# Performance work log

Hardware: AMD Instinct MI355X
Metric: run time of the kernel (lower is better)

Reference implementation:

```python
import jax, jax.numpy as jnp
import numpy as np

B, NJ, NM = 64, 30, 20
N = NJ * NM          # 600 operation nodes per FJSP instance
IN_DIM, H = 2, 128


def _bn(h):
    # torch BatchNorm1d in training mode, gamma=1/beta=0 (module init), stats over all nodes
    m = h.mean(axis=(0, 1))
    v = h.var(axis=(0, 1))
    return (h - m) / jnp.sqrt(v + 1e-5)


def setup_inputs() -> dict:
    key = jax.random.key(0)
    ks = jax.random.split(key, 20)
    x = jax.random.normal(ks[0], (B, N, IN_DIM), jnp.float32)
    graph_pool = jnp.full((B, N), 1.0 / N, jnp.float32)   # average graph pooling weights
    padded_nei = jnp.zeros((1,), jnp.int32)               # unused (sum pooling path)
    adj = (jax.random.uniform(ks[1], (B, N, N)) < 0.01).astype(jnp.float32)
    adj = jnp.minimum(adj + jnp.eye(N, dtype=jnp.float32)[None], 1.0)  # self-loops
    candidate = jax.random.randint(ks[2], (B, NJ), 0, N)
    a_index = jax.random.randint(ks[3], (B,), 0, NJ)
    mask = jax.random.uniform(ks[4], (B, NJ)) < 0.2
    mask = mask.at[jnp.arange(B), a_index].set(False)     # chosen action never masked
    mask_mch = jax.random.uniform(ks[5], (B, N, NM)) < 0.3
    dur = jax.random.uniform(ks[6], (B, N, NM), dtype=jnp.float32)
    old_action = jax.random.randint(ks[7], (B,), 0, N)
    mch_pool = jax.random.normal(ks[8], (B, H), jnp.float32)

    def w(k, i, o):
        return jax.random.normal(k, (i, o), jnp.float32) * (1.0 / np.sqrt(i))

    z = lambda n: jnp.zeros((n,), jnp.float32)            # biases init to 0 in module
    return dict(
        x=x, graph_pool=graph_pool, padded_nei=padded_nei, adj=adj,
        candidate=candidate, mask=mask, mask_mch=mask_mch, dur=dur,
        a_index=a_index, old_action=old_action, mch_pool=mch_pool,
        W1_0=w(ks[9], IN_DIM, H), b1_0=z(H), W2_0=w(ks[10], H, H), b2_0=z(H),
        W1_1=w(ks[11], H, H), b1_1=z(H), W2_1=w(ks[12], H, H), b2_1=z(H),
        Wa1=w(ks[13], 3 * H, H), ba1=z(H), Wa2=w(ks[14], H, H), ba2=z(H),
        Wa3=w(ks[15], H, 1), ba3=z(1),
        Wc1=w(ks[16], H, H), bc1=z(H), Wc2=w(ks[17], H, 1), bc2=z(1),
    )


def reference(x, graph_pool, padded_nei, adj, candidate, mask, mask_mch, dur,
              a_index, old_action, mch_pool,
              W1_0, b1_0, W2_0, b2_0, W1_1, b1_1, W2_1, b2_1,
              Wa1, ba1, Wa2, ba2, Wa3, ba3, Wc1, bc1, Wc2, bc2):
    # --- GIN encoder: num_layers-1 = 2 message-passing layers, sum pooling ---
    h = x
    for (W1, b1, W2, b2) in ((W1_0, b1_0, W2_0, b2_0), (W1_1, b1_1, W2_1, b2_1)):
        pooled = jnp.einsum('bnm,bmd->bnd', adj, h)         # neighbor sum (adj has self-loops)
        h1 = jax.nn.relu(_bn(pooled @ W1 + b1))             # MLP hidden (BN inside MLP)
        h = jax.nn.relu(_bn(h1 @ W2 + b2))                  # layer BN + relu
    h_nodes = h                                             # [B, N, H]
    h_pooled = jnp.einsum('bn,bnd->bd', graph_pool, h_nodes)  # [B, H]

    # --- gather candidate features, concat pooled contexts ---
    cand_feat = jnp.take_along_axis(h_nodes, candidate[:, :, None], axis=1)  # [B, NJ, H]
    concat = jnp.concatenate([
        cand_feat,
        jnp.broadcast_to(h_pooled[:, None, :], cand_feat.shape),
        jnp.broadcast_to(mch_pool[:, None, :], cand_feat.shape)], axis=-1)   # [B, NJ, 3H]

    # --- MLPActor(3 layers, tanh) ---
    a = jnp.tanh(concat @ Wa1 + ba1)
    a = jnp.tanh(a @ Wa2 + ba2)
    scores = (a @ Wa3 + ba3).squeeze(-1) * 10.0             # [B, NJ]
    scores = jnp.where(mask, -jnp.inf, scores)
    logpi = jax.nn.log_softmax(scores, axis=1)
    pi = jnp.exp(logpi)
    log_a = jnp.take_along_axis(logpi, a_index[:, None], axis=1)[:, 0]
    entropy = -jnp.sum(jnp.where(pi > 0, pi * logpi, 0.0), axis=1)

    # --- gather action-dependent tensors (detached in torch) ---
    b_idx = jnp.arange(B)
    action_node = dur[b_idx, old_action]                    # [B, NM]
    action_feature = h_nodes[b_idx, old_action]             # [B, H]
    mask_mch_action = mask_mch[b_idx, old_action][:, None, :]  # [B, 1, NM]

    # --- MLPCritic(2 layers, tanh) ---
    v = jnp.tanh(h_pooled @ Wc1 + bc1) @ Wc2 + bc2          # [B, 1]

    sg = jax.lax.stop_gradient
    return (entropy, v, log_a, sg(action_node), sg(action_feature),
            mask_mch_action, sg(h_pooled))
```

## Files before the change

kernel.cpp:

```cpp
#include <hip/hip_runtime.h>
#include <hip/hip_bf16.h>

#define BB 64
#define NJ 30
#define NM 20
#define NN 600
#define HH 128
#define NROWS (BB*NN)
#define CAP 48

typedef __attribute__((ext_vector_type(8))) short short8;
typedef __attribute__((ext_vector_type(4))) float f32x4;

#define STATS_B   0
#define HPOOL_B   4096
#define FLAGS_B   36864
#define ZERO_B    36880
#define WTB_B     37120
#define SCORES_B  135424
#define NBRCNT_B  143104
#define NBRIDX_B  296704
#define POOLED0_B 7669504
#define T1_B      7976704
#define P1_B      27637504

#define OUT_ENT   0
#define OUT_V     64
#define OUT_LOGA  128
#define OUT_ANODE 192
#define OUT_AFEAT 1472
#define OUT_MMCH  9664
#define OUT_HPOOL 10944

__device__ __forceinline__ bool mask_at(const void* p, int layout, long i) {
    if (layout == 2) return ((const float*)p)[i] != 0.f;
    if (layout == 1) return ((const unsigned char*)p)[i] != 0;
    return ((const int*)p)[i] != 0;
}

__device__ __forceinline__ short bf16rne(float f) {
    unsigned u = __float_as_uint(f);
    return (short)((u + 0x7fffu + ((u >> 16) & 1u)) >> 16);
}
__device__ __forceinline__ float bf2f(unsigned h) {
    return __uint_as_float(h << 16);
}
__device__ __forceinline__ unsigned packbf(float a, float b) {
    return ((unsigned)(unsigned short)bf16rne(a)) |
           (((unsigned)(unsigned short)bf16rne(b)) << 16);
}

__global__ __launch_bounds__(256) void k_sparse(const float* __restrict__ adj,
                                                const float* __restrict__ x,
                                                int* __restrict__ nbr_cnt,
                                                int* __restrict__ nbr_idx,
                                                float* __restrict__ pooled0,
                                                const void* mask_p, const void* maskmch_p,
                                                int* flags,
                                                const float* __restrict__ Wa,
                                                const float* __restrict__ Wb,
                                                const float* __restrict__ Wc,
                                                unsigned short* __restrict__ wT) {
    int bid = blockIdx.x;
    int tid = threadIdx.x;
    if (bid < 289) {
        if (bid >= 97) {
            int bid2 = bid - 97;
            int mat = bid2 >> 6;
            int idx = ((bid2 & 63) << 8) + tid;
            const float* W = mat == 0 ? Wa : (mat == 1 ? Wb : Wc);
            int k = idx >> 7, c = idx & 127;
            wT[mat * 16384 + c * HH + k] = (unsigned short)bf16rne(W[idx]);
        } else {
            unsigned agg = 0;
            int which;
            if (bid == 0) {
                which = 0;
                const unsigned* p = (const unsigned*)mask_p;
                unsigned w0 = (tid < 480) ? p[tid] : 0u;
                unsigned w1 = (tid + 256 < 480) ? p[tid + 256] : 0u;
                agg = w0 | w1;
            } else {
                which = 1;
                const unsigned* p = (const unsigned*)maskmch_p + (size_t)(bid - 1) * 200;
                agg = (tid < 200) ? p[tid] : 0u;
            }
            int f = 0;
            if (((agg >> 24) & 0xffu) == 0x3fu) f |= 1;
            if ((((agg >> 8) & 0xffu) == 1u) || (((agg >> 16) & 0xffu) == 1u) ||
                (((agg >> 24) & 0xffu) == 1u)) f |= 2;
#pragma unroll
            for (int off = 1; off < 64; off <<= 1) f |= __shfl_xor(f, off);
            if ((tid & 63) == 0 && f) atomicOr(&flags[which], f);
        }
    }

    int wrow = bid * 4 + (tid >> 6);
    int lane = tid & 63;
    int b = wrow / NN;
    const float4* arow = (const float4*)(adj + (size_t)wrow * NN);
    int* irow = nbr_idx + (size_t)wrow * CAP;
    const float* xb = x + (size_t)b * NN * 2;
    float4 vv[3];
    vv[0] = arow[lane];
    vv[1] = arow[64 + lane];
    vv[2] = (128 + lane < 150) ? arow[128 + lane] : make_float4(0.f, 0.f, 0.f, 0.f);
    int cnt = 0;
    float p0 = 0.f, p1 = 0.f;
#pragma unroll
    for (int it = 0; it < 3; ++it) {
        float4 v = vv[it];
        int col0 = it * 256 + lane * 4;
        bool m0 = v.x != 0.f, m1 = v.y != 0.f, m2 = v.z != 0.f, m3 = v.w != 0.f;
        int c_lane = (int)m0 + (int)m1 + (int)m2 + (int)m3;
        int inc = c_lane;
#pragma unroll
        for (int off = 1; off < 64; off <<= 1) {
            int t = __shfl_up(inc, off);
            if (lane >= off) inc += t;
        }
        int pos = cnt + inc - c_lane;
        if (m0) {
            if (pos < CAP) irow[pos] = col0;
            float2 xv = *(const float2*)&xb[col0 * 2];
            p0 += xv.x; p1 += xv.y; ++pos;
        }
        if (m1) {
            if (pos < CAP) irow[pos] = col0 + 1;
            float2 xv = *(const float2*)&xb[(col0 + 1) * 2];
            p0 += xv.x; p1 += xv.y; ++pos;
        }
        if (m2) {
            if (pos < CAP) irow[pos] = col0 + 2;
            float2 xv = *(const float2*)&xb[(col0 + 2) * 2];
            p0 += xv.x; p1 += xv.y; ++pos;
        }
        if (m3) {
            if (pos < CAP) irow[pos] = col0 + 3;
            float2 xv = *(const float2*)&xb[(col0 + 3) * 2];
            p0 += xv.x; p1 += xv.y; ++pos;
        }
        cnt += __shfl(inc, 63);
    }
#pragma unroll
    for (int off = 1; off < 64; off <<= 1) {
        p0 += __shfl_xor(p0, off);
        p1 += __shfl_xor(p1, off);
    }
    if (lane == 0) {
        nbr_cnt[wrow] = cnt < CAP ? cnt : CAP;
        pooled0[(size_t)wrow * 2]     = p0;
        pooled0[(size_t)wrow * 2 + 1] = p1;
    }
}

__global__ __launch_bounds__(256) void k_p0stats(const float* __restrict__ pooled0,
                                                 float* __restrict__ out5) {
    __shared__ float red[4][5];
    int i = blockIdx.x * 256 + threadIdx.x;
    float p0 = pooled0[(size_t)i * 2], p1 = pooled0[(size_t)i * 2 + 1];
    float v[5] = {p0, p1, p0 * p0, p1 * p1, p0 * p1};
#pragma unroll
    for (int j = 0; j < 5; ++j)
#pragma unroll
        for (int off = 1; off < 64; off <<= 1) v[j] += __shfl_xor(v[j], off);
    int lane = threadIdx.x & 63, w = threadIdx.x >> 6;
    if (lane == 0)
#pragma unroll
        for (int j = 0; j < 5; ++j) red[w][j] = v[j];
    __syncthreads();
    if (threadIdx.x == 0)
#pragma unroll
        for (int j = 0; j < 5; ++j)
            atomicAdd(&out5[j], red[0][j] + red[1][j] + red[2][j] + red[3][j]);
}

template<int MODE>
__global__ __launch_bounds__(256) void k_stage(const void* __restrict__ t_in_v,
                                               const float* __restrict__ pooled0,
                                               const float* __restrict__ W1,
                                               const unsigned short* __restrict__ wT,
                                               const float* __restrict__ stats_in,
                                               unsigned short* __restrict__ t_out,
                                               float* __restrict__ stats_out) {
    __shared__ float sm_mean[HH], sm_inv[HH];
    __shared__ float smS[4][32], smQ[4][32];
    int tid = threadIdx.x;
    if (MODE == 0 && tid < HH) {
        float S0 = stats_in[0], S1 = stats_in[1], Q0 = stats_in[2], Q1 = stats_in[3], P01 = stats_in[4];
        float w0 = W1[tid], w1 = W1[HH + tid];
        float m = (S0 * w0 + S1 * w1) * (1.f / NROWS);
        float eq = (Q0 * w0 * w0 + Q1 * w1 * w1 + 2.f * P01 * w0 * w1) * (1.f / NROWS);
        sm_mean[tid] = m;
        sm_inv[tid] = 1.f / sqrtf(eq - m * m + 1e-5f);
    }
    if (MODE == 1 && tid < HH) {
        float s = stats_in[tid], q = stats_in[HH + tid];
        float m = s * (1.f / NROWS);
        sm_mean[tid] = m;
        sm_inv[tid] = 1.f / sqrtf(q * (1.f / NROWS) - m * m + 1e-5f);
    }
    if (MODE != 2) __syncthreads();

    const unsigned short* tin = (const unsigned short*)t_in_v;
    int lane = tid & 63, wave = tid >> 6;
    int r16 = lane & 15, kg = lane >> 4;
    int rowbase = (blockIdx.x >> 2) * 64 + wave * 16;
    int colq = blockIdx.x & 3;

    f32x4 acc[2];
#pragma unroll
    for (int t = 0; t < 2; ++t)
#pragma unroll
        for (int i = 0; i < 4; ++i) acc[t][i] = 0.f;

    float p0 = 0.f, p1 = 0.f;
    if (MODE == 0) {
        p0 = pooled0[(size_t)(rowbase + r16) * 2];
        p1 = pooled0[(size_t)(rowbase + r16) * 2 + 1];
    }

#pragma unroll
    for (int ks = 0; ks < 4; ++ks) {
        int kb = ks * 32 + kg * 8;
        short8 afr;
        if (MODE == 2) {
            afr = *(const short8*)&tin[(size_t)(rowbase + r16) * HH + kb];
        } else {
            float av[8];
            if (MODE == 0) {
                float4 wa0 = *(const float4*)&W1[kb];
                float4 wa1 = *(const float4*)&W1[kb + 4];
                float4 wb0 = *(const float4*)&W1[HH + kb];
                float4 wb1 = *(const float4*)&W1[HH + kb + 4];
                av[0] = p0 * wa0.x + p1 * wb0.x; av[1] = p0 * wa0.y + p1 * wb0.y;
                av[2] = p0 * wa0.z + p1 * wb0.z; av[3] = p0 * wa0.w + p1 * wb0.w;
                av[4] = p0 * wa1.x + p1 * wb1.x; av[5] = p0 * wa1.y + p1 * wb1.y;
                av[6] = p0 * wa1.z + p1 * wb1.z; av[7] = p0 * wa1.w + p1 * wb1.w;
            } else {
                short8 raw = *(const short8*)&tin[(size_t)(rowbase + r16) * HH + kb];
#pragma unroll
                for (int j = 0; j < 8; ++j) av[j] = bf2f((unsigned short)raw[j]);
            }
            float4 m0 = *(const float4*)&sm_mean[kb];
            float4 m1 = *(const float4*)&sm_mean[kb + 4];
            float4 i0 = *(const float4*)&sm_inv[kb];
            float4 i1 = *(const float4*)&sm_inv[kb + 4];
            av[0] = fmaxf((av[0] - m0.x) * i0.x, 0.f);
            av[1] = fmaxf((av[1] - m0.y) * i0.y, 0.f);
            av[2] = fmaxf((av[2] - m0.z) * i0.z, 0.f);
            av[3] = fmaxf((av[3] - m0.w) * i0.w, 0.f);
            av[4] = fmaxf((av[4] - m1.x) * i1.x, 0.f);
            av[5] = fmaxf((av[5] - m1.y) * i1.y, 0.f);
            av[6] = fmaxf((av[6] - m1.z) * i1.z, 0.f);
            av[7] = fmaxf((av[7] - m1.w) * i1.w, 0.f);
#pragma unroll
            for (int j = 0; j < 8; ++j) afr[j] = bf16rne(av[j]);
        }
#pragma unroll
        for (int t = 0; t < 2; ++t) {
            short8 bfr = *(const short8*)&wT[(size_t)((colq * 2 + t) * 16 + r16) * HH + kb];
            acc[t] = __builtin_amdgcn_mfma_f32_16x16x32_bf16(afr, bfr, acc[t], 0, 0, 0);
        }
    }

#pragma unroll
    for (int t = 0; t < 2; ++t) {
        int lc = t * 16 + r16;
        int col = colq * 32 + lc;
        float s = 0.f, q = 0.f;
#pragma unroll
        for (int i = 0; i < 4; ++i) {
            float v = acc[t][i];
            t_out[(size_t)(rowbase + kg * 4 + i) * HH + col] = (unsigned short)bf16rne(v);
            s += v; q += v * v;
        }
        s += __shfl_xor(s, 16); q += __shfl_xor(q, 16);
        s += __shfl_xor(s, 32); q += __shfl_xor(q, 32);
        if (kg == 0) { smS[wave][lc] = s; smQ[wave][lc] = q; }
    }
    __syncthreads();
    if (tid < 32) {
        int col = colq * 32 + tid;
        atomicAdd(&stats_out[col],      smS[0][tid] + smS[1][tid] + smS[2][tid] + smS[3][tid]);
        atomicAdd(&stats_out[HH + col], smQ[0][tid] + smQ[1][tid] + smQ[2][tid] + smQ[3][tid]);
    }
}

__global__ __launch_bounds__(256) void k_pool1(const unsigned short* __restrict__ t1,
                                               const int* __restrict__ nbr_cnt,
                                               const int* __restrict__ nbr_idx,
                                               const float* __restrict__ stats1,
                                               unsigned short* __restrict__ pooled1) {
    __shared__ float sm_mean[HH], sm_inv[HH];
    int tid = threadIdx.x;
    if (tid < HH) {
        float s = stats1[tid], q = stats1[HH + tid];
        float m = s * (1.f / NROWS);
        sm_mean[tid] = m;
        sm_inv[tid] = 1.f / sqrtf(q * (1.f / NROWS) - m * m + 1e-5f);
    }
    __syncthreads();
    int c4 = tid & 31, rl = tid >> 5;
    int row = blockIdx.x * 8 + rl;
    int b = row / NN;
    float4 mm = *(const float4*)&sm_mean[c4 * 4];
    float4 iv = *(const float4*)&sm_inv[c4 * 4];
    int cnt = nbr_cnt[row];
    const int* ir = nbr_idx + (size_t)row * CAP;
    const unsigned short* tb = t1 + (size_t)b * NN * HH;
    float a0 = 0.f, a1 = 0.f, a2 = 0.f, a3 = 0.f;
    int i = 0;
    for (; i + 1 < cnt; i += 2) {
        int m0 = ir[i], m1 = ir[i + 1];
        uint2 w0 = *(const uint2*)&tb[(size_t)m0 * HH + c4 * 4];
        uint2 w1 = *(const uint2*)&tb[(size_t)m1 * HH + c4 * 4];
        a0 += fmaxf((bf2f(w0.x & 0xffffu) - mm.x) * iv.x, 0.f)
            + fmaxf((bf2f(w1.x & 0xffffu) - mm.x) * iv.x, 0.f);
        a1 += fmaxf((bf2f(w0.x >> 16)     - mm.y) * iv.y, 0.f)
            + fmaxf((bf2f(w1.x >> 16)     - mm.y) * iv.y, 0.f);
        a2 += fmaxf((bf2f(w0.y & 0xffffu) - mm.z) * iv.z, 0.f)
            + fmaxf((bf2f(w1.y & 0xffffu) - mm.z) * iv.z, 0.f);
        a3 += fmaxf((bf2f(w0.y >> 16)     - mm.w) * iv.w, 0.f)
            + fmaxf((bf2f(w1.y >> 16)     - mm.w) * iv.w, 0.f);
    }
    if (i < cnt) {
        int m0 = ir[i];
        uint2 w0 = *(const uint2*)&tb[(size_t)m0 * HH + c4 * 4];
        a0 += fmaxf((bf2f(w0.x & 0xffffu) - mm.x) * iv.x, 0.f);
        a1 += fmaxf((bf2f(w0.x >> 16)     - mm.y) * iv.y, 0.f);
        a2 += fmaxf((bf2f(w0.y & 0xffffu) - mm.z) * iv.z, 0.f);
        a3 += fmaxf((bf2f(w0.y >> 16)     - mm.w) * iv.w, 0.f);
    }
    uint2 o;
    o.x = packbf(a0, a1);
    o.y = packbf(a2, a3);
    *(uint2*)&pooled1[(size_t)row * HH + c4 * 4] = o;
}

__global__ __launch_bounds__(256) void k_hpool(const unsigned short* __restrict__ t3,
                                               const float* __restrict__ gp,
                                               const float* __restrict__ stats3,
                                               float* __restrict__ hpool) {
    __shared__ float sm_mean[HH], sm_inv[HH];
    __shared__ float red[8][HH];
    int tid = threadIdx.x;
    if (tid < HH) {
        float s = stats3[tid], q = stats3[HH + tid];
        float m = s * (1.f / NROWS);
        sm_mean[tid] = m;
        sm_inv[tid] = 1.f / sqrtf(q * (1.f / NROWS) - m * m + 1e-5f);
    }
    __syncthreads();
    int b = blockIdx.x >> 3, chunk = blockIdx.x & 7;
    int c4 = tid & 31, rl = tid >> 5;
    float4 mm = *(const float4*)&sm_mean[c4 * 4];
    float4 iv = *(const float4*)&sm_inv[c4 * 4];
    float a0 = 0.f, a1 = 0.f, a2 = 0.f, a3 = 0.f;
    int nend = chunk * 75 + 75;
    for (int n = chunk * 75 + rl; n < nend; n += 8) {
        float w = gp[b * NN + n];
        uint2 t = *(const uint2*)&t3[((size_t)b * NN + n) * HH + c4 * 4];
        a0 += w * fmaxf((bf2f(t.x & 0xffffu) - mm.x) * iv.x, 0.f);
        a1 += w * fmaxf((bf2f(t.x >> 16)     - mm.y) * iv.y, 0.f);
        a2 += w * fmaxf((bf2f(t.y & 0xffffu) - mm.z) * iv.z, 0.f);
        a3 += w * fmaxf((bf2f(t.y >> 16)     - mm.w) * iv.w, 0.f);
    }
    *(float4*)&red[rl][c4 * 4] = make_float4(a0, a1, a2, a3);
    __syncthreads();
    if (tid < HH) {
        float s = 0.f;
#pragma unroll
        for (int g = 0; g < 8; ++g) s += red[g][tid];
        atomicAdd(&hpool[b * HH + tid], s);
    }
}

__global__ __launch_bounds__(256) void k_actor(const unsigned short* __restrict__ t3,
                                               const int* __restrict__ cand,
                                               const float* __restrict__ hpool,
                                               const float* __restrict__ mch,
                                               const float* __restrict__ stats3,
                                               const float* __restrict__ Wa1,
                                               const float* __restrict__ ba1,
                                               const float* __restrict__ Wa2,
                                               const float* __restrict__ ba2,
                                               const float* __restrict__ Wa3,
                                               const float* __restrict__ ba3,
                                               float* __restrict__ scores) {
    __shared__ float sh_c[8 * 384];
    __shared__ float sh_a1[8 * HH];
    __shared__ float sred[8][HH];
    int tid = threadIdx.x;
    int rbase = blockIdx.x * 8;
    int c = tid & 127, slot = tid >> 7;

    float mean_c, inv_c;
    {
        float s = stats3[c], q = stats3[HH + c];
        float m = s * (1.f / NROWS);
        mean_c = m;
        inv_c = 1.f / sqrtf(q * (1.f / NROWS) - m * m + 1e-5f);
    }
#pragma unroll
    for (int rr = 0; rr < 4; ++rr) {
        int r = slot * 4 + rr;
        int row = rbase + r;
        int b = row / NJ;
        int cd = cand[row];
        float v = bf2f(t3[((size_t)b * NN + cd) * HH + c]);
        sh_c[r * 384 + c]       = fmaxf((v - mean_c) * inv_c, 0.f);
        sh_c[r * 384 + 128 + c] = hpool[b * HH + c];
        sh_c[r * 384 + 256 + c] = mch[b * HH + c];
    }
    __syncthreads();

    float acc[4] = {0.f, 0.f, 0.f, 0.f};
    for (int k = 0; k < 384; ++k) {
        float w = Wa1[(size_t)k * HH + c];
#pragma unroll
        for (int rr = 0; rr < 4; ++rr)
            acc[rr] += sh_c[(slot * 4 + rr) * 384 + k] * w;
    }
    float bb = ba1[c];
#pragma unroll
    for (int rr = 0; rr < 4; ++rr)
        sh_a1[(slot * 4 + rr) * HH + c] = tanhf(acc[rr] + bb);
    __syncthreads();

    float acc2[4] = {0.f, 0.f, 0.f, 0.f};
    for (int k = 0; k < HH; ++k) {
        float w = Wa2[(size_t)k * HH + c];
#pragma unroll
        for (int rr = 0; rr < 4; ++rr)
            acc2[rr] += sh_a1[(slot * 4 + rr) * HH + k] * w;
    }
    float w3 = Wa3[c], bb2 = ba2[c];
#pragma unroll
    for (int rr = 0; rr < 4; ++rr)
        sred[slot * 4 + rr][c] = tanhf(acc2[rr] + bb2) * w3;
    __syncthreads();
    int r = tid >> 5, l32 = tid & 31;
    float v = sred[r][l32] + sred[r][l32 + 32] + sred[r][l32 + 64] + sred[r][l32 + 96];
    v += __shfl_xor(v, 1); v += __shfl_xor(v, 2); v += __shfl_xor(v, 4);
    v += __shfl_xor(v, 8); v += __shfl_xor(v, 16);
    if (l32 == 0) scores[rbase + r] = 10.f * (v + ba3[0]);
}

__global__ __launch_bounds__(128) void k_final(const unsigned short* __restrict__ t3,
                                               const float* __restrict__ stats3,
                                               const float* __restrict__ hpool,
                                               const float* __restrict__ scores,
                                               const void* __restrict__ mask_p,
                                               const void* __restrict__ maskmch_p,
                                               const int* __restrict__ flags,
                                               const float* __restrict__ dur,
                                               const int* __restrict__ a_index,
                                               const int* __restrict__ old_action,
                                               const float* __restrict__ Wc1,
                                               const float* __restrict__ bc1,
                                               const float* __restrict__ Wc2,
                                               const float* __restrict__ bc2,
                                               float* __restrict__ out) {
    __shared__ float sm_mean[HH], sm_inv[HH], sh_hp[HH], sh_red[HH];
    __shared__ float sh_s[32], sh_lp[32];
    __shared__ int sh_m[32];
    int b = blockIdx.x, t = threadIdx.x;
    {
        float s = stats3[t], q = stats3[HH + t];
        float m = s * (1.f / NROWS);
        sm_mean[t] = m;
        sm_inv[t] = 1.f / sqrtf(q * (1.f / NROWS) - m * m + 1e-5f);
    }
    sh_hp[t] = hpool[b * HH + t];
    __syncthreads();

    float acc = bc1[t];
    for (int k = 0; k < HH; ++k) acc += sh_hp[k] * Wc1[k * HH + t];
    sh_red[t] = tanhf(acc) * Wc2[t];
    __syncthreads();
    for (int st = 64; st > 0; st >>= 1) {
        if (t < st) sh_red[t] += sh_red[t + st];
        __syncthreads();
    }
    if (t == 0) out[OUT_V + b] = sh_red[0] + bc2[0];

    int fA = flags[0], fB = flags[1];
    int layA = (fA & 1) ? 2 : ((fA & 2) ? 1 : 0);
    int layB = (fB & 1) ? 2 : ((fB & 2) ? 1 : 0);
    if (t < NJ) {
        sh_s[t] = scores[b * NJ + t];
        sh_m[t] = mask_at(mask_p, layA, (long)b * NJ + t) ? 1 : 0;
    }
    __syncthreads();
    if (t == 0) {
        float mx = -1e30f;
        for (int j = 0; j < NJ; ++j)
            if (!sh_m[j] && sh_s[j] > mx) mx = sh_s[j];
        float sum = 0.f;
        for (int j = 0; j < NJ; ++j)
            if (!sh_m[j]) sum += expf(sh_s[j] - mx);
        float lse = mx + logf(sum);
        float ent = 0.f;
        for (int j = 0; j < NJ; ++j) {
            if (!sh_m[j]) {
                float lp = sh_s[j] - lse;
                sh_lp[j] = lp;
                float pi = expf(lp);
                if (pi > 0.f) ent -= pi * lp;
            }
        }
        out[OUT_ENT + b] = ent;
        out[OUT_LOGA + b] = sh_lp[a_index[b]];
    }

    int old = old_action[b];
    if (t < NM) {
        out[OUT_ANODE + b * NM + t] = dur[((size_t)b * NN + old) * NM + t];
        out[OUT_MMCH + b * NM + t] =
            mask_at(maskmch_p, layB, ((size_t)b * NN + old) * NM + t) ? 1.f : 0.f;
    }
    {
        float v = bf2f(t3[((size_t)b * NN + old) * HH + t]);
        out[OUT_AFEAT + b * HH + t] = fmaxf((v - sm_mean[t]) * sm_inv[t], 0.f);
        out[OUT_HPOOL + b * HH + t] = sh_hp[t];
    }
}

extern "C" void kernel_launch(void* const* d_in, const int* in_sizes, int n_in,
                              void* d_out, int out_size, void* d_ws, size_t ws_size,
                              hipStream_t stream) {
    (void)in_sizes; (void)n_in; (void)out_size; (void)ws_size;
    const float* x         = (const float*)d_in[0];
    const float* gp        = (const float*)d_in[1];
    const float* adj       = (const float*)d_in[3];
    const int*   cand      = (const int*)d_in[4];
    const void*  mask_p    = d_in[5];
    const void*  maskmch_p = d_in[6];
    const float* dur       = (const float*)d_in[7];
    const int*   a_index   = (const int*)d_in[8];
    const int*   old_act   = (const int*)d_in[9];
    const float* mch_pool  = (const float*)d_in[10];
    const float* W1_0 = (const float*)d_in[11];
    const float* W2_0 = (const float*)d_in[13];
    const float* W1_1 = (const float*)d_in[15];
    const float* W2_1 = (const float*)d_in[17];
    const float* Wa1  = (const float*)d_in[19];
    const float* ba1  = (const float*)d_in[20];
    const float* Wa2  = (const float*)d_in[21];
    const float* ba2  = (const float*)d_in[22];
    const float* Wa3  = (const float*)d_in[23];
    const float* ba3  = (const float*)d_in[24];
    const float* Wc1  = (const float*)d_in[25];
    const float* bc1  = (const float*)d_in[26];
    const float* Wc2  = (const float*)d_in[27];
    const float* bc2  = (const float*)d_in[28];

    char* ws = (char*)d_ws;
    float* stats   = (float*)(ws + STATS_B);
    float* hpool   = (float*)(ws + HPOOL_B);
    int*   flags   = (int*)(ws + FLAGS_B);
    unsigned short* wtb = (unsigned short*)(ws + WTB_B);
    float* scores  = (float*)(ws + SCORES_B);
    int*   nbr_cnt = (int*)(ws + NBRCNT_B);
    int*   nbr_idx = (int*)(ws + NBRIDX_B);
    float* pooled0 = (float*)(ws + POOLED0_B);
    unsigned short* t1_16 = (unsigned short*)(ws + T1_B);
    unsigned short* p1_16 = (unsigned short*)(ws + P1_B);
    float* out     = (float*)d_out;

    hipMemsetAsync(ws, 0, ZERO_B, stream);
    k_sparse<<<NROWS / 4, 256, 0, stream>>>(adj, x, nbr_cnt, nbr_idx, pooled0,
                                            mask_p, maskmch_p, flags, W2_0, W1_1, W2_1, wtb);
    k_p0stats<<<NROWS / 256, 256, 0, stream>>>(pooled0, stats);
    k_stage<0><<<2400, 256, 0, stream>>>(nullptr, pooled0, W1_0, wtb, stats, t1_16, stats + 256);
    k_pool1<<<NROWS / 8, 256, 0, stream>>>(t1_16, nbr_cnt, nbr_idx, stats + 256, p1_16);
    k_stage<2><<<2400, 256, 0, stream>>>(p1_16, nullptr, nullptr, wtb + 16384, stats, t1_16, stats + 512);
    k_stage<1><<<2400, 256, 0, stream>>>(t1_16, nullptr, nullptr, wtb + 32768, stats + 512,
                                         p1_16, stats + 768);
    k_hpool<<<BB * 8, 256, 0, stream>>>(p1_16, gp, stats + 768, hpool);
    k_actor<<<240, 256, 0, stream>>>(p1_16, cand, hpool, mch_pool, stats + 768,
                                     Wa1, ba1, Wa2, ba2, Wa3, ba3, scores);
    k_final<<<BB, 128, 0, stream>>>(p1_16, stats + 768, hpool, scores, mask_p, maskmch_p, flags,
                                    dur, a_index, old_act, Wc1, bc1, Wc2, bc2, out);
}
```

Baseline: 352.5 us.

## Fuse all pipeline stages into one cooperative persistent kernel with grid syncs

```diff
diff --git a/kernel.cpp b/kernel.cpp
--- a/kernel.cpp
+++ b/kernel.cpp
@@ -1,5 +1,8 @@
 #include <hip/hip_runtime.h>
 #include <hip/hip_bf16.h>
+#include <hip/hip_cooperative_groups.h>
+
+namespace cg = cooperative_groups;
 
 #define BB 64
 #define NJ 30
@@ -8,6 +11,7 @@
 #define HH 128
 #define NROWS (BB*NN)
 #define CAP 48
+#define GRID 1024
 
 typedef __attribute__((ext_vector_type(8))) short short8;
 typedef __attribute__((ext_vector_type(4))) float f32x4;
@@ -49,6 +53,7 @@
     return ((unsigned)(unsigned short)bf16rne(a)) |
            (((unsigned)(unsigned short)bf16rne(b)) << 16);
 }
+
 
 __global__ __launch_bounds__(256) void k_sparse(const float* __restrict__ adj,
                                                 const float* __restrict__ x,
@@ -527,6 +532,513 @@
     }
 }
 
+
+template<int MODE>
+__device__ __forceinline__ void stage_phase(
+    int bid, int tid, float* smem,
+    const unsigned short* __restrict__ tin,
+    const float* __restrict__ pooled0,
+    const float* __restrict__ W1,
+    const unsigned short* __restrict__ wT,
+    const float* __restrict__ stats_in,
+    unsigned short* __restrict__ t_out,
+    float* __restrict__ stats_out)
+{
+    float* sm_mean = smem;
+    float* sm_inv  = smem + HH;
+    float* smS     = smem + 2 * HH;
+    float* smQ     = smem + 2 * HH + 128;
+
+    if (MODE == 0 && tid < HH) {
+        float S0 = stats_in[0], S1 = stats_in[1], Q0 = stats_in[2], Q1 = stats_in[3], P01 = stats_in[4];
+        float w0 = W1[tid], w1 = W1[HH + tid];
+        float m = (S0 * w0 + S1 * w1) * (1.f / NROWS);
+        float eq = (Q0 * w0 * w0 + Q1 * w1 * w1 + 2.f * P01 * w0 * w1) * (1.f / NROWS);
+        sm_mean[tid] = m;
+        sm_inv[tid] = 1.f / sqrtf(eq - m * m + 1e-5f);
+    }
+    if (MODE == 1 && tid < HH) {
+        float s = stats_in[tid], q = stats_in[HH + tid];
+        float m = s * (1.f / NROWS);
+        sm_mean[tid] = m;
+        sm_inv[tid] = 1.f / sqrtf(q * (1.f / NROWS) - m * m + 1e-5f);
+    }
+    __syncthreads();
+
+    int lane = tid & 63, wave = tid >> 6;
+    int r16 = lane & 15, kg = lane >> 4;
+
+    for (int vb = bid; vb < 2400; vb += GRID) {
+        int rowbase = (vb >> 2) * 64 + wave * 16;
+        int colq = vb & 3;
+
+        f32x4 acc[2];
+#pragma unroll
+        for (int t = 0; t < 2; ++t)
+#pragma unroll
+            for (int i = 0; i < 4; ++i) acc[t][i] = 0.f;
+
+        float p0 = 0.f, p1 = 0.f;
+        if (MODE == 0) {
+            p0 = pooled0[(size_t)(rowbase + r16) * 2];
+            p1 = pooled0[(size_t)(rowbase + r16) * 2 + 1];
+        }
+
+#pragma unroll
+        for (int ks = 0; ks < 4; ++ks) {
+            int kb = ks * 32 + kg * 8;
+            short8 afr;
+            if (MODE == 2) {
+                afr = *(const short8*)&tin[(size_t)(rowbase + r16) * HH + kb];
+            } else {
+                float av[8];
+                if (MODE == 0) {
+                    float4 wa0 = *(const float4*)&W1[kb];
+                    float4 wa1 = *(const float4*)&W1[kb + 4];
+                    float4 wb0 = *(const float4*)&W1[HH + kb];
+                    float4 wb1 = *(const float4*)&W1[HH + kb + 4];
+                    av[0] = p0 * wa0.x + p1 * wb0.x; av[1] = p0 * wa0.y + p1 * wb0.y;
+                    av[2] = p0 * wa0.z + p1 * wb0.z; av[3] = p0 * wa0.w + p1 * wb0.w;
+                    av[4] = p0 * wa1.x + p1 * wb1.x; av[5] = p0 * wa1.y + p1 * wb1.y;
+                    av[6] = p0 * wa1.z + p1 * wb1.z; av[7] = p0 * wa1.w + p1 * wb1.w;
+                } else {
+                    short8 raw = *(const short8*)&tin[(size_t)(rowbase + r16) * HH + kb];
+#pragma unroll
+                    for (int j = 0; j < 8; ++j) av[j] = bf2f((unsigned short)raw[j]);
+                }
+                float4 m0 = *(const float4*)&sm_mean[kb];
+                float4 m1 = *(const float4*)&sm_mean[kb + 4];
+                float4 i0 = *(const float4*)&sm_inv[kb];
+                float4 i1 = *(const float4*)&sm_inv[kb + 4];
+                av[0] = fmaxf((av[0] - m0.x) * i0.x, 0.f);
+                av[1] = fmaxf((av[1] - m0.y) * i0.y, 0.f);
+                av[2] = fmaxf((av[2] - m0.z) * i0.z, 0.f);
+                av[3] = fmaxf((av[3] - m0.w) * i0.w, 0.f);
+                av[4] = fmaxf((av[4] - m1.x) * i1.x, 0.f);
+                av[5] = fmaxf((av[5] - m1.y) * i1.y, 0.f);
+                av[6] = fmaxf((av[6] - m1.z) * i1.z, 0.f);
+                av[7] = fmaxf((av[7] - m1.w) * i1.w, 0.f);
+#pragma unroll
+                for (int j = 0; j < 8; ++j) afr[j] = bf16rne(av[j]);
+            }
+#pragma unroll
+            for (int t = 0; t < 2; ++t) {
+                short8 bfr = *(const short8*)&wT[(size_t)((colq * 2 + t) * 16 + r16) * HH + kb];
+                acc[t] = __builtin_amdgcn_mfma_f32_16x16x32_bf16(afr, bfr, acc[t], 0, 0, 0);
+            }
+        }
+
+#pragma unroll
+        for (int t = 0; t < 2; ++t) {
+            int lc = t * 16 + r16;
+            int col = colq * 32 + lc;
+            float s = 0.f, q = 0.f;
+#pragma unroll
+            for (int i = 0; i < 4; ++i) {
+                float v = acc[t][i];
+                t_out[(size_t)(rowbase + kg * 4 + i) * HH + col] = (unsigned short)bf16rne(v);
+                s += v; q += v * v;
+            }
+            s += __shfl_xor(s, 16); q += __shfl_xor(q, 16);
+            s += __shfl_xor(s, 32); q += __shfl_xor(q, 32);
+            if (kg == 0) { smS[wave * 32 + lc] = s; smQ[wave * 32 + lc] = q; }
+        }
+        __syncthreads();
+        if (tid < 32) {
+            int col = colq * 32 + tid;
+            atomicAdd(&stats_out[col],
+                      smS[tid] + smS[32 + tid] + smS[64 + tid] + smS[96 + tid]);
+            atomicAdd(&stats_out[HH + col],
+                      smQ[tid] + smQ[32 + tid] + smQ[64 + tid] + smQ[96 + tid]);
+        }
+        __syncthreads();
+    }
+}
+
+__global__ __launch_bounds__(256, 4) void k_mega(
+    const float* __restrict__ adj,
+    const float* __restrict__ x,
+    const float* __restrict__ gp,
+    const int* __restrict__ cand,
+    const void* __restrict__ mask_p,
+    const void* __restrict__ maskmch_p,
+    const float* __restrict__ dur,
+    const int* __restrict__ a_index,
+    const int* __restrict__ old_action,
+    const float* __restrict__ mch,
+    const float* __restrict__ W1_0,
+    const float* __restrict__ W2_0,
+    const float* __restrict__ W1_1,
+    const float* __restrict__ W2_1,
+    const float* __restrict__ Wa1, const float* __restrict__ ba1,
+    const float* __restrict__ Wa2, const float* __restrict__ ba2,
+    const float* __restrict__ Wa3, const float* __restrict__ ba3,
+    const float* __restrict__ Wc1, const float* __restrict__ bc1,
+    const float* __restrict__ Wc2, const float* __restrict__ bc2,
+    char* __restrict__ ws,
+    float* __restrict__ out)
+{
+    cg::grid_group grid = cg::this_grid();
+
+    float* stats   = (float*)(ws + STATS_B);
+    float* hpool   = (float*)(ws + HPOOL_B);
+    int*   flags   = (int*)(ws + FLAGS_B);
+    unsigned short* wtb = (unsigned short*)(ws + WTB_B);
+    float* scores  = (float*)(ws + SCORES_B);
+    int*   nbr_cnt = (int*)(ws + NBRCNT_B);
+    int*   nbr_idx = (int*)(ws + NBRIDX_B);
+    float* pooled0 = (float*)(ws + POOLED0_B);
+    unsigned short* t1_16 = (unsigned short*)(ws + T1_B);
+    unsigned short* p1_16 = (unsigned short*)(ws + P1_B);
+
+    __shared__ float smem[5120];
+
+    const int bid = blockIdx.x;
+    const int tid = threadIdx.x;
+    const int lane = tid & 63;
+    const int wave = tid >> 6;
+
+    {
+        float s0 = 0.f, s1 = 0.f, s2 = 0.f, s3 = 0.f, s4 = 0.f;
+        for (int vb = bid; vb < NROWS / 4; vb += GRID) {
+            if (vb < 289) {
+                if (vb >= 97) {
+                    int bid2 = vb - 97;
+                    int mat = bid2 >> 6;
+                    int idx = ((bid2 & 63) << 8) + tid;
+                    const float* W = mat == 0 ? W2_0 : (mat == 1 ? W1_1 : W2_1);
+                    int k = idx >> 7, c = idx & 127;
+                    wtb[mat * 16384 + c * HH + k] = (unsigned short)bf16rne(W[idx]);
+                } else {
+                    unsigned agg = 0;
+                    int which;
+                    if (vb == 0) {
+                        which = 0;
+                        const unsigned* p = (const unsigned*)mask_p;
+                        unsigned w0 = (tid < 480) ? p[tid] : 0u;
+                        unsigned w1 = (tid + 256 < 480) ? p[tid + 256] : 0u;
+                        agg = w0 | w1;
+                    } else {
+                        which = 1;
+                        const unsigned* p = (const unsigned*)maskmch_p + (size_t)(vb - 1) * 200;
+                        agg = (tid < 200) ? p[tid] : 0u;
+                    }
+                    int f = 0;
+                    if (((agg >> 24) & 0xffu) == 0x3fu) f |= 1;
+                    if ((((agg >> 8) & 0xffu) == 1u) || (((agg >> 16) & 0xffu) == 1u) ||
+                        (((agg >> 24) & 0xffu) == 1u)) f |= 2;
+#pragma unroll
+                    for (int off = 1; off < 64; off <<= 1) f |= __shfl_xor(f, off);
+                    if (lane == 0 && f) atomicOr(&flags[which], f);
+                }
+            }
+            int wrow = vb * 4 + wave;
+            int b = wrow / NN;
+            const float4* arow = (const float4*)(adj + (size_t)wrow * NN);
+            int* irow = nbr_idx + (size_t)wrow * CAP;
+            const float* xb = x + (size_t)b * NN * 2;
+            float4 vv[3];
+            vv[0] = arow[lane];
+            vv[1] = arow[64 + lane];
+            vv[2] = (128 + lane < 150) ? arow[128 + lane] : make_float4(0.f, 0.f, 0.f, 0.f);
+            int cnt = 0;
+            float p0 = 0.f, p1 = 0.f;
+#pragma unroll
+            for (int it = 0; it < 3; ++it) {
+                float4 v = vv[it];
+                int col0 = it * 256 + lane * 4;
+                bool m0 = v.x != 0.f, m1 = v.y != 0.f, m2 = v.z != 0.f, m3 = v.w != 0.f;
+                int c_lane = (int)m0 + (int)m1 + (int)m2 + (int)m3;
+                int inc = c_lane;
+#pragma unroll
+                for (int off = 1; off < 64; off <<= 1) {
+                    int t = __shfl_up(inc, off);
+                    if (lane >= off) inc += t;
+                }
+                int pos = cnt + inc - c_lane;
+                if (m0) {
+                    if (pos < CAP) irow[pos] = col0;
+                    float2 xv = *(const float2*)&xb[col0 * 2];
+                    p0 += xv.x; p1 += xv.y; ++pos;
+                }
+                if (m1) {
+                    if (pos < CAP) irow[pos] = col0 + 1;
+                    float2 xv = *(const float2*)&xb[(col0 + 1) * 2];
+                    p0 += xv.x; p1 += xv.y; ++pos;
+                }
+                if (m2) {
+                    if (pos < CAP) irow[pos] = col0 + 2;
+                    float2 xv = *(const float2*)&xb[(col0 + 2) * 2];
+                    p0 += xv.x; p1 += xv.y; ++pos;
+                }
+                if (m3) {
+                    if (pos < CAP) irow[pos] = col0 + 3;
+                    float2 xv = *(const float2*)&xb[(col0 + 3) * 2];
+                    p0 += xv.x; p1 += xv.y; ++pos;
+                }
+                cnt += __shfl(inc, 63);
+            }
+#pragma unroll
+            for (int off = 1; off < 64; off <<= 1) {
+                p0 += __shfl_xor(p0, off);
+                p1 += __shfl_xor(p1, off);
+            }
+            if (lane == 0) {
+                nbr_cnt[wrow] = cnt < CAP ? cnt : CAP;
+                pooled0[(size_t)wrow * 2]     = p0;
+                pooled0[(size_t)wrow * 2 + 1] = p1;
+            }
+            s0 += p0; s1 += p1; s2 += p0 * p0; s3 += p1 * p1; s4 += p0 * p1;
+        }
+        if (lane == 0) {
+            smem[wave * 5 + 0] = s0; smem[wave * 5 + 1] = s1; smem[wave * 5 + 2] = s2;
+            smem[wave * 5 + 3] = s3; smem[wave * 5 + 4] = s4;
+        }
+        __syncthreads();
+        if (tid < 5)
+            atomicAdd(&stats[tid], smem[tid] + smem[5 + tid] + smem[10 + tid] + smem[15 + tid]);
+    }
+    grid.sync();
+
+    stage_phase<0>(bid, tid, smem, nullptr, pooled0, W1_0, wtb, stats, t1_16, stats + 256);
+    grid.sync();
+
+    {
+        float* sm_mean = smem;
+        float* sm_inv  = smem + HH;
+        if (tid < HH) {
+            float s = stats[256 + tid], q = stats[256 + HH + tid];
+            float m = s * (1.f / NROWS);
+            sm_mean[tid] = m;
+            sm_inv[tid] = 1.f / sqrtf(q * (1.f / NROWS) - m * m + 1e-5f);
+        }
+        __syncthreads();
+        int c4 = tid & 31, rl = tid >> 5;
+        float4 mm = *(const float4*)&sm_mean[c4 * 4];
+        float4 iv = *(const float4*)&sm_inv[c4 * 4];
+        for (int vb = bid; vb < NROWS / 8; vb += GRID) {
+            int row = vb * 8 + rl;
+            int b = row / NN;
+            int cnt = nbr_cnt[row];
+            const int* ir = nbr_idx + (size_t)row * CAP;
+            const unsigned short* tb = t1_16 + (size_t)b * NN * HH;
+            float a0 = 0.f, a1 = 0.f, a2 = 0.f, a3 = 0.f;
+            int i = 0;
+            for (; i + 1 < cnt; i += 2) {
+                int m0 = ir[i], m1 = ir[i + 1];
+                uint2 w0 = *(const uint2*)&tb[(size_t)m0 * HH + c4 * 4];
+                uint2 w1 = *(const uint2*)&tb[(size_t)m1 * HH + c4 * 4];
+                a0 += fmaxf((bf2f(w0.x & 0xffffu) - mm.x) * iv.x, 0.f)
+                    + fmaxf((bf2f(w1.x & 0xffffu) - mm.x) * iv.x, 0.f);
+                a1 += fmaxf((bf2f(w0.x >> 16)     - mm.y) * iv.y, 0.f)
+                    + fmaxf((bf2f(w1.x >> 16)     - mm.y) * iv.y, 0.f);
+                a2 += fmaxf((bf2f(w0.y & 0xffffu) - mm.z) * iv.z, 0.f)
+                    + fmaxf((bf2f(w1.y & 0xffffu) - mm.z) * iv.z, 0.f);
+                a3 += fmaxf((bf2f(w0.y >> 16)     - mm.w) * iv.w, 0.f)
+                    + fmaxf((bf2f(w1.y >> 16)     - mm.w) * iv.w, 0.f);
+            }
+            if (i < cnt) {
+                int m0 = ir[i];
+                uint2 w0 = *(const uint2*)&tb[(size_t)m0 * HH + c4 * 4];
+                a0 += fmaxf((bf2f(w0.x & 0xffffu) - mm.x) * iv.x, 0.f);
+                a1 += fmaxf((bf2f(w0.x >> 16)     - mm.y) * iv.y, 0.f);
+                a2 += fmaxf((bf2f(w0.y & 0xffffu) - mm.z) * iv.z, 0.f);
+                a3 += fmaxf((bf2f(w0.y >> 16)     - mm.w) * iv.w, 0.f);
+            }
+            uint2 o;
+            o.x = packbf(a0, a1);
+            o.y = packbf(a2, a3);
+            *(uint2*)&p1_16[(size_t)row * HH + c4 * 4] = o;
+        }
+    }
+    grid.sync();
+
+    stage_phase<2>(bid, tid, smem, p1_16, nullptr, nullptr, wtb + 16384, nullptr,
+                   t1_16, stats + 512);
+    grid.sync();
+
+    stage_phase<1>(bid, tid, smem, t1_16, nullptr, nullptr, wtb + 32768, stats + 512,
+                   p1_16, stats + 768);
+    grid.sync();
+
+    {
+        const float* stats3 = stats + 768;
+        if (bid < BB * 8) {
+            float* sm_mean = smem;
+            float* sm_inv  = smem + HH;
+            float* red     = smem + 2 * HH;
+            if (tid < HH) {
+                float s = stats3[tid], q = stats3[HH + tid];
+                float m = s * (1.f / NROWS);
+                sm_mean[tid] = m;
+                sm_inv[tid] = 1.f / sqrtf(q * (1.f / NROWS) - m * m + 1e-5f);
+            }
+            __syncthreads();
+            int b = bid >> 3, chunk = bid & 7;
+            int c4 = tid & 31, rl = tid >> 5;
+            float4 mm = *(const float4*)&sm_mean[c4 * 4];
+            float4 iv = *(const float4*)&sm_inv[c4 * 4];
+            float a0 = 0.f, a1 = 0.f, a2 = 0.f, a3 = 0.f;
+            int nend = chunk * 75 + 75;
+            for (int n = chunk * 75 + rl; n < nend; n += 8) {
+                float w = gp[b * NN + n];
+                uint2 t = *(const uint2*)&p1_16[((size_t)b * NN + n) * HH + c4 * 4];
+                a0 += w * fmaxf((bf2f(t.x & 0xffffu) - mm.x) * iv.x, 0.f);
+                a1 += w * fmaxf((bf2f(t.x >> 16)     - mm.y) * iv.y, 0.f);
+                a2 += w * fmaxf((bf2f(t.y & 0xffffu) - mm.z) * iv.z, 0.f);
+                a3 += w * fmaxf((bf2f(t.y >> 16)     - mm.w) * iv.w, 0.f);
+            }
+            *(float4*)&red[rl * HH + c4 * 4] = make_float4(a0, a1, a2, a3);
+            __syncthreads();
+            if (tid < HH) {
+                float s = 0.f;
+#pragma unroll
+                for (int g = 0; g < 8; ++g) s += red[g * HH + tid];
+                atomicAdd(&hpool[b * HH + tid], s);
+            }
+        }
+    }
+    grid.sync();
+
+    {
+        const float* stats3 = stats + 768;
+        if (bid < 240) {
+            float* sh_c  = smem;
+            float* sh_a1 = smem + 3072;
+            float* sred  = smem + 4096;
+            int rbase = bid * 8;
+            int c = tid & 127, slot = tid >> 7;
+
+            float mean_c, inv_c;
+            {
+                float s = stats3[c], q = stats3[HH + c];
+                float m = s * (1.f / NROWS);
+                mean_c = m;
+                inv_c = 1.f / sqrtf(q * (1.f / NROWS) - m * m + 1e-5f);
+            }
+#pragma unroll
+            for (int rr = 0; rr < 4; ++rr) {
+                int r = slot * 4 + rr;
+                int row = rbase + r;
+                int b = row / NJ;
+                int cd = cand[row];
+                float v = bf2f(p1_16[((size_t)b * NN + cd) * HH + c]);
+                sh_c[r * 384 + c]       = fmaxf((v - mean_c) * inv_c, 0.f);
+                sh_c[r * 384 + 128 + c] = hpool[b * HH + c];
+                sh_c[r * 384 + 256 + c] = mch[b * HH + c];
+            }
+            __syncthreads();
+
+            float acc[4] = {0.f, 0.f, 0.f, 0.f};
+            for (int k = 0; k < 384; ++k) {
+                float w = Wa1[(size_t)k * HH + c];
+#pragma unroll
+                for (int rr = 0; rr < 4; ++rr)
+                    acc[rr] += sh_c[(slot * 4 + rr) * 384 + k] * w;
+            }
+            float bb = ba1[c];
+#pragma unroll
+            for (int rr = 0; rr < 4; ++rr)
+                sh_a1[(slot * 4 + rr) * HH + c] = tanhf(acc[rr] + bb);
+            __syncthreads();
+
+            float acc2[4] = {0.f, 0.f, 0.f, 0.f};
+            for (int k = 0; k < HH; ++k) {
+                float w = Wa2[(size_t)k * HH + c];
+#pragma unroll
+                for (int rr = 0; rr < 4; ++rr)
+                    acc2[rr] += sh_a1[(slot * 4 + rr) * HH + k] * w;
+            }
+            float w3 = Wa3[c], bb2 = ba2[c];
+#pragma unroll
+            for (int rr = 0; rr < 4; ++rr)
+                sred[(slot * 4 + rr) * HH + c] = tanhf(acc2[rr] + bb2) * w3;
+            __syncthreads();
+            int r = tid >> 5, l32 = tid & 31;
+            float v = sred[r * HH + l32] + sred[r * HH + l32 + 32]
+                    + sred[r * HH + l32 + 64] + sred[r * HH + l32 + 96];
+            v += __shfl_xor(v, 1); v += __shfl_xor(v, 2); v += __shfl_xor(v, 4);
+            v += __shfl_xor(v, 8); v += __shfl_xor(v, 16);
+            if (l32 == 0) scores[rbase + r] = 10.f * (v + ba3[0]);
+        }
+    }
+    grid.sync();
+
+    {
+        const float* stats3 = stats + 768;
+        if (bid < BB) {
+            float* sm_mean = smem;
+            float* sm_inv  = smem + 128;
+            float* sh_hp   = smem + 256;
+            float* sh_red  = smem + 384;
+            float* sh_s    = smem + 512;
+            float* sh_lp   = smem + 544;
+            int*   sh_m    = (int*)(smem + 576);
+            int b = bid, t = tid;
+            if (t < HH) {
+                float s = stats3[t], q = stats3[HH + t];
+                float m = s * (1.f / NROWS);
+                sm_mean[t] = m;
+                sm_inv[t] = 1.f / sqrtf(q * (1.f / NROWS) - m * m + 1e-5f);
+                sh_hp[t] = hpool[b * HH + t];
+            }
+            __syncthreads();
+            if (t < HH) {
+                float acc = bc1[t];
+                for (int k = 0; k < HH; ++k) acc += sh_hp[k] * Wc1[k * HH + t];
+                sh_red[t] = tanhf(acc) * Wc2[t];
+            }
+            __syncthreads();
+            for (int st = 64; st > 0; st >>= 1) {
+                if (t < st) sh_red[t] += sh_red[t + st];
+                __syncthreads();
+            }
+            if (t == 0) out[OUT_V + b] = sh_red[0] + bc2[0];
+
+            int fA = flags[0], fB = flags[1];
+            int layA = (fA & 1) ? 2 : ((fA & 2) ? 1 : 0);
+            int layB = (fB & 1) ? 2 : ((fB & 2) ? 1 : 0);
+            if (t < NJ) {
+                sh_s[t] = scores[b * NJ + t];
+                sh_m[t] = mask_at(mask_p, layA, (long)b * NJ + t) ? 1 : 0;
+            }
+            __syncthreads();
+            if (t == 0) {
+                float mx = -1e30f;
+                for (int j = 0; j < NJ; ++j)
+                    if (!sh_m[j] && sh_s[j] > mx) mx = sh_s[j];
+                float sum = 0.f;
+                for (int j = 0; j < NJ; ++j)
+                    if (!sh_m[j]) sum += expf(sh_s[j] - mx);
+                float lse = mx + logf(sum);
+                float ent = 0.f;
+                for (int j = 0; j < NJ; ++j) {
+                    if (!sh_m[j]) {
+                        float lp = sh_s[j] - lse;
+                        sh_lp[j] = lp;
+                        float pi = expf(lp);
+                        if (pi > 0.f) ent -= pi * lp;
+                    }
+                }
+                out[OUT_ENT + b] = ent;
+                out[OUT_LOGA + b] = sh_lp[a_index[b]];
+            }
+
+            int old = old_action[b];
+            if (t < NM) {
+                out[OUT_ANODE + b * NM + t] = dur[((size_t)b * NN + old) * NM + t];
+                out[OUT_MMCH + b * NM + t] =
+                    mask_at(maskmch_p, layB, ((size_t)b * NN + old) * NM + t) ? 1.f : 0.f;
+            }
+            if (t < HH) {
+                float v = bf2f(p1_16[((size_t)b * NN + old) * HH + t]);
+                out[OUT_AFEAT + b * HH + t] = fmaxf((v - sm_mean[t]) * sm_inv[t], 0.f);
+                out[OUT_HPOOL + b * HH + t] = sh_hp[t];
+            }
+        }
+    }
+}
+
 extern "C" void kernel_launch(void* const* d_in, const int* in_sizes, int n_in,
                               void* d_out, int out_size, void* d_ws, size_t ws_size,
                               hipStream_t stream) {
@@ -570,17 +1082,32 @@
     float* out     = (float*)d_out;
 
     hipMemsetAsync(ws, 0, ZERO_B, stream);
-    k_sparse<<<NROWS / 4, 256, 0, stream>>>(adj, x, nbr_cnt, nbr_idx, pooled0,
-                                            mask_p, maskmch_p, flags, W2_0, W1_1, W2_1, wtb);
-    k_p0stats<<<NROWS / 256, 256, 0, stream>>>(pooled0, stats);
-    k_stage<0><<<2400, 256, 0, stream>>>(nullptr, pooled0, W1_0, wtb, stats, t1_16, stats + 256);
-    k_pool1<<<NROWS / 8, 256, 0, stream>>>(t1_16, nbr_cnt, nbr_idx, stats + 256, p1_16);
-    k_stage<2><<<2400, 256, 0, stream>>>(p1_16, nullptr, nullptr, wtb + 16384, stats, t1_16, stats + 512);
-    k_stage<1><<<2400, 256, 0, stream>>>(t1_16, nullptr, nullptr, wtb + 32768, stats + 512,
-                                         p1_16, stats + 768);
-    k_hpool<<<BB * 8, 256, 0, stream>>>(p1_16, gp, stats + 768, hpool);
-    k_actor<<<240, 256, 0, stream>>>(p1_16, cand, hpool, mch_pool, stats + 768,
-                                     Wa1, ba1, Wa2, ba2, Wa3, ba3, scores);
-    k_final<<<BB, 128, 0, stream>>>(p1_16, stats + 768, hpool, scores, mask_p, maskmch_p, flags,
-                                    dur, a_index, old_act, Wc1, bc1, Wc2, bc2, out);
-}
+
+    void* kargs[] = {
+        (void*)&adj, (void*)&x, (void*)&gp, (void*)&cand,
+        (void*)&mask_p, (void*)&maskmch_p, (void*)&dur,
+        (void*)&a_index, (void*)&old_act, (void*)&mch_pool,
+        (void*)&W1_0, (void*)&W2_0, (void*)&W1_1, (void*)&W2_1,
+        (void*)&Wa1, (void*)&ba1, (void*)&Wa2, (void*)&ba2, (void*)&Wa3, (void*)&ba3,
+        (void*)&Wc1, (void*)&bc1, (void*)&Wc2, (void*)&bc2,
+        (void*)&ws, (void*)&out
+    };
+    hipError_t e = hipLaunchCooperativeKernel((const void*)k_mega, dim3(GRID), dim3(256),
+                                              kargs, 0, stream);
+    if (e != hipSuccess) {
+        (void)hipGetLastError();
+        k_sparse<<<NROWS / 4, 256, 0, stream>>>(adj, x, nbr_cnt, nbr_idx, pooled0,
+                                                mask_p, maskmch_p, flags, W2_0, W1_1, W2_1, wtb);
+        k_p0stats<<<NROWS / 256, 256, 0, stream>>>(pooled0, stats);
+        k_stage<0><<<2400, 256, 0, stream>>>(nullptr, pooled0, W1_0, wtb, stats, t1_16, stats + 256);
+        k_pool1<<<NROWS / 8, 256, 0, stream>>>(t1_16, nbr_cnt, nbr_idx, stats + 256, p1_16);
+        k_stage<2><<<2400, 256, 0, stream>>>(p1_16, nullptr, nullptr, wtb + 16384, stats, t1_16, stats + 512);
+        k_stage<1><<<2400, 256, 0, stream>>>(t1_16, nullptr, nullptr, wtb + 32768, stats + 512,
+                                             p1_16, stats + 768);
+        k_hpool<<<BB * 8, 256, 0, stream>>>(p1_16, gp, stats + 768, hpool);
+        k_actor<<<240, 256, 0, stream>>>(p1_16, cand, hpool, mch_pool, stats + 768,
+                                         Wa1, ba1, Wa2, ba2, Wa3, ba3, scores);
+        k_final<<<BB, 128, 0, stream>>>(p1_16, stats + 768, hpool, scores, mask_p, maskmch_p, flags,
+                                        dur, a_index, old_act, Wc1, bc1, Wc2, bc2, out);
+    }
+}
```

Result: slower. 1.162 ms (+229.8%).
